# Optimization experiments

Measured on AMD Instinct MI355X. Metric: run time of the kernel, lower is better.

## Reference

```python
import jax, jax.numpy as jnp
import numpy as np

D = 0.035          # propagation distance (m)
LAMBDA = 5.32e-07  # wavelength (m)
RES = 64           # field resolution
N_LAYERS = 3
M = 50             # Monte-Carlo screens
BATCH = 128
NUM_CLASSES = 10
W0 = 0.01          # beam waist (m)
L_COH = 2e-3       # coherence length (m)
DX = 1e-06         # pixel pitch (m)
K = 2.0 * np.pi / LAMBDA


def _transfer_fn():
    # Angular-spectrum Fresnel transfer function H (host-side constant)
    f = np.fft.fftfreq(RES, DX)
    FX, FY = np.meshgrid(f, f)
    H = np.exp(1j * K * D) * np.exp(-1j * np.pi * LAMBDA * D * (FX ** 2 + FY ** 2))
    return jnp.asarray(H, dtype=jnp.complex64)


def setup_inputs() -> dict:
    key = jax.random.key(0)
    kx, k1, k2, kp, kw, kb = jax.random.split(key, 6)
    x = jax.random.uniform(kx, (BATCH, 1, RES, RES), dtype=jnp.float32)
    # Gauss-Schell complex random screens T_m (paper Eq.6), precomputed since they are random draws
    Cm = jax.random.normal(k1, (M, RES, RES), dtype=jnp.float32) + 1j * jax.random.normal(k2, (M, RES, RES), dtype=jnp.float32)
    v = np.fft.fftfreq(RES, 1.0 / RES)
    VX, VY = np.meshgrid(v, v)
    p = 2.0 * np.pi * L_COH ** 2 * np.exp(-2.0 * np.pi ** 2 * L_COH ** 2 * (VX ** 2 + VY ** 2))
    Tm = jnp.fft.ifft2(Cm * jnp.asarray(np.sqrt(p), dtype=jnp.float32))
    g = np.linspace(-W0 / 2, W0 / 2, RES)
    X, Y = np.meshgrid(g, g)
    gauss = jnp.asarray(np.exp(-(X ** 2 + Y ** 2) / W0 ** 2), dtype=jnp.float32)
    Tm = Tm * gauss
    Tm = Tm / jnp.max(jnp.abs(Tm), axis=(1, 2), keepdims=True)
    Tm = Tm.astype(jnp.complex64)
    phase_masks = jax.random.normal(kp, (N_LAYERS, RES, RES), dtype=jnp.float32) * 0.1
    fc_w = jax.random.normal(kw, (NUM_CLASSES, RES * RES), dtype=jnp.float32) * (1.0 / RES)
    fc_b = jax.random.normal(kb, (NUM_CLASSES,), dtype=jnp.float32) * 0.01
    return {"x": x, "screens_re": jnp.real(Tm), "screens_im": jnp.imag(Tm),
            "phase_masks": phase_masks, "fc_w": fc_w, "fc_b": fc_b}


def reference(x, screens_re, screens_im, phase_masks, fc_w, fc_b):
    H = _transfer_fn()  # [RES, RES] complex64
    screens = (screens_re + 1j * screens_im).astype(jnp.complex64)  # [M, r, r]
    # field: [M, B, r, r] -- all Monte-Carlo screens batched at once
    field = x[:, 0].astype(jnp.complex64)[None, :, :, :] * screens[:, None, :, :]
    for l in range(phase_masks.shape[0]):  # small fixed layer count
        field = field * jnp.exp(1j * phase_masks[l]).astype(jnp.complex64)
        field = jnp.fft.ifft2(jnp.fft.fft2(field) * H)
    avg_intensity = jnp.mean(jnp.abs(field) ** 2, axis=0)  # [B, r, r]
    feat = avg_intensity.reshape(avg_intensity.shape[0], -1)
    return feat @ fc_w.T + fc_b
```

## Files before the change

kernel.cpp:

```cpp
#include <hip/hip_runtime.h>
#include <math.h>

#define NM   50
#define NB   128
#define NL   3
#define NCLS 10

#define PI_D        3.14159265358979323846264338327950288
#define TWO_PI_D    6.28318530717958647692528676655900577
#define INV_2PI_D   0.159154943091895335768883763372514362
#define LAMBDA_D    5.32e-07
#define DIST_D      0.035
#define PLD_D       (PI_D * LAMBDA_D * DIST_D)
#define KD_D        (TWO_PI_D / LAMBDA_D * DIST_D)

typedef float f2 __attribute__((ext_vector_type(2)));

__device__ __forceinline__ f2 mkf2(float a, float b) { f2 r; r.x = a; r.y = b; return r; }

__device__ __forceinline__ int sw(int r, int c) {
    return r * 64 + (c ^ (((r & 3) << 2) ^ ((c >> 4) & 3)));
}
#define QS(r) ((((r) & 15)) << 1)

__device__ __forceinline__ constexpr int rev4(int i) {
    return ((i & 1) << 3) | ((i & 2) << 1) | ((i & 4) >> 1) | ((i & 8) >> 3);
}

__device__ __forceinline__ float dppx1(float v) {
    return __int_as_float(__builtin_amdgcn_mov_dpp(__float_as_int(v), 0xB1, 0xF, 0xF, true));
}
__device__ __forceinline__ float dppx2(float v) {
    return __int_as_float(__builtin_amdgcn_mov_dpp(__float_as_int(v), 0x4E, 0xF, 0xF, true));
}

__device__ __forceinline__ f2 cmul(f2 a, f2 w) {
    return a * w.x + a.yx * mkf2(-w.y, w.y);
}
__device__ __forceinline__ f2 cmulc(f2 a, f2 w) {
    return a * w.x + a.yx * mkf2(w.y, -w.y);
}

__device__ __forceinline__ constexpr float c16t(int tw) {
    return (tw == 1) ? 0.923879532511286756f : (tw == 2) ? 0.707106781186547524f :
           (tw == 3) ? 0.382683432365089772f : (tw == 5) ? -0.382683432365089772f :
           (tw == 6) ? -0.707106781186547524f : (tw == 7) ? -0.923879532511286756f : 1.0f;
}
__device__ __forceinline__ constexpr float s16t(int tw) {
    return (tw == 1) ? 0.382683432365089772f : (tw == 2) ? 0.707106781186547524f :
           (tw == 3) ? 0.923879532511286756f : (tw == 5) ? 0.923879532511286756f :
           (tw == 6) ? 0.707106781186547524f : (tw == 7) ? 0.382683432365089772f : 0.0f;
}

__device__ __forceinline__ void dif16_fwd(f2* x) {
#pragma unroll
    for (int len = 8; len >= 1; len >>= 1) {
#pragma unroll
        for (int base = 0; base < 16; base += 2 * len) {
#pragma unroll
            for (int j = 0; j < len; j++) {
                const int i0 = base + j, i1 = i0 + len;
                const int tw = j * (8 / len);
                f2 a = x[i0], b = x[i1];
                x[i0] = a + b;
                f2 d = a - b;
                if (tw == 0)      { x[i1] = d; }
                else if (tw == 4) { x[i1] = mkf2(d.y, -d.x); }
                else {
                    const float c = c16t(tw), s = s16t(tw);
                    x[i1] = d * c + d.yx * mkf2(s, -s);
                }
            }
        }
    }
}

__device__ __forceinline__ void dit16_inv(f2* x) {
#pragma unroll
    for (int len = 1; len <= 8; len <<= 1) {
#pragma unroll
        for (int base = 0; base < 16; base += 2 * len) {
#pragma unroll
            for (int j = 0; j < len; j++) {
                const int i0 = base + j, i1 = i0 + len;
                const int tw = j * (8 / len);
                f2 a = x[i0], b = x[i1];
                if (tw == 4)      { b = mkf2(-b.y, b.x); }
                else if (tw != 0) {
                    const float c = c16t(tw), s = s16t(tw);
                    b = b * c + b.yx * mkf2(-s, s);
                }
                x[i0] = a + b;
                x[i1] = a - b;
            }
        }
    }
}

__device__ __forceinline__ void quad_fwd(f2* x, float s1, float s2, bool l3) {
#pragma unroll
    for (int i = 0; i < 16; i++) {
        f2 p = mkf2(dppx2(x[i].x), dppx2(x[i].y));
        f2 r = x[i] * s2 + p;
        f2 r2 = l3 ? mkf2(r.y, -r.x) : r;
        f2 q = mkf2(dppx1(r2.x), dppx1(r2.y));
        x[i] = r2 * s1 + q;
    }
}

__device__ __forceinline__ void quad_inv(f2* x, float s1, float s2, bool l3) {
#pragma unroll
    for (int i = 0; i < 16; i++) {
        f2 p = mkf2(dppx1(x[i].x), dppx1(x[i].y));
        f2 r = x[i] * s1 + p;
        f2 r2 = l3 ? mkf2(-r.y, r.x) : r;
        f2 q = mkf2(dppx2(r2.x), dppx2(r2.y));
        x[i] = r2 * s2 + q;
    }
}

__device__ __forceinline__ void fwd64(f2* x, const f2* w64t, int t, float s1, float s2, bool l3) {
    dif16_fwd(x);
#pragma unroll
    for (int i = 1; i < 16; i++) x[i] = cmulc(x[i], w64t[t * rev4(i)]);
    quad_fwd(x, s1, s2, l3);
}
__device__ __forceinline__ void inv64(f2* x, const f2* w64t, int t, float s1, float s2, bool l3) {
    quad_inv(x, s1, s2, l3);
#pragma unroll
    for (int i = 1; i < 16; i++) x[i] = cmul(x[i], w64t[t * rev4(i)]);
    dit16_inv(x);
}

__global__ __launch_bounds__(256) void donn_main(
    const float* __restrict__ x,
    const float* __restrict__ sre,
    const float* __restrict__ sim,
    const float* __restrict__ phase,
    const float* __restrict__ fcw,
    const float* __restrict__ fcb,
    float* __restrict__ out)
{
    __shared__ f2 xb2[4096];
    __shared__ f2 w64t[64];
    __shared__ f2 hx2[64], hy2[64];

    const int tid = threadIdx.x;
    const int bid = blockIdx.x;
    const int b = bid & (NB - 1);
    const int m = bid >> 7;
    const int g = tid >> 2, t = tid & 3;
    const int sig = ((t & 1) << 1) | (t >> 1);
    const bool l3 = (t == 3);
    const float s1 = (t & 1) ? -1.f : 1.f;
    const float s2 = (t & 2) ? -1.f : 1.f;

    if (tid < 64) {
        float s, c;
        __sincosf((float)tid * (float)(TWO_PI_D / 64.0), &s, &c);
        w64t[tid] = mkf2(c, s);
        double f = (double)((tid < 32) ? tid : tid - 64) * 15625.0;
        double phd = -PLD_D * f * f;
        double r1 = phd - TWO_PI_D * rint(phd * INV_2PI_D);
        hx2[tid] = mkf2(cosf((float)r1), sinf((float)r1));
        double r2 = phd + KD_D;
        r2 = r2 - TWO_PI_D * rint(r2 * INV_2PI_D);
        hy2[tid] = mkf2(cosf((float)r2) * (1.0f / 4096.0f),
                        sinf((float)r2) * (1.0f / 4096.0f));
    }

    f2 X[16];
    {
        const float* xb = x   + b * 4096 + g * 64 + t;
        const float* sr = sre + m * 4096 + g * 64 + t;
        const float* si = sim + m * 4096 + g * 64 + t;
#pragma unroll
        for (int j = 0; j < 16; j++) {
            float xv = xb[4 * j];
            X[j].x = xv * sr[4 * j];
            X[j].y = xv * si[4 * j];
        }
    }
    __syncthreads();

#pragma unroll 1
    for (int l = 0; l < NL; l++) {
        const float* ph = phase + l * 4096 + g * 64 + t;
#pragma unroll
        for (int j = 0; j < 16; j++) {
            float s, c;
            __sincosf(ph[4 * j], &s, &c);
            X[j] = cmul(X[j], mkf2(c, s));
        }
        fwd64(X, w64t, t, s1, s2, l3);
#pragma unroll
        for (int i = 0; i < 16; i++) {
            const int kk = rev4(i) + 16 * sig;
            X[i] = cmul(X[i], hx2[kk]);
        }
#pragma unroll
        for (int i = 0; i < 16; i++) {
            const int kk = rev4(i) + 16 * sig;
            xb2[sw(g, kk)] = X[i];
        }
        __syncthreads();
#pragma unroll
        for (int j = 0; j < 16; j++)
            X[j] = xb2[sw(4 * j + t, g)];
        fwd64(X, w64t, t, s1, s2, l3);
#pragma unroll
        for (int i = 0; i < 16; i++) {
            const int kk = rev4(i) + 16 * sig;
            X[i] = cmul(X[i], hy2[kk]);
        }
        inv64(X, w64t, t, s1, s2, l3);
#pragma unroll
        for (int j = 0; j < 16; j++)
            xb2[sw(4 * j + t, g)] = X[j];
        __syncthreads();
#pragma unroll
        for (int i = 0; i < 16; i++) {
            const int kk = rev4(i) + 16 * sig;
            X[i] = xb2[sw(g, kk)];
        }
        inv64(X, w64t, t, s1, s2, l3);
    }

    __syncthreads();
    float* xbf = (float*)xb2;
    const int qsg = QS(g);
#pragma unroll
    for (int j = 0; j < 16; j++) {
        const int c0 = 4 * j + t;
        xbf[g * 64 + (c0 ^ qsg)] = fmaf(X[j].x, X[j].x, X[j].y * X[j].y);
    }
    __syncthreads();

    float ivl[16];
#pragma unroll
    for (int i = 0; i < 16; i++) {
        const int e = i * 256 + tid;
        const int r = e >> 6, c = e & 63;
        ivl[i] = xbf[r * 64 + (c ^ QS(r))];
    }
    float part[NCLS];
#pragma unroll
    for (int c2 = 0; c2 < NCLS; c2++) part[c2] = 0.f;
#pragma unroll
    for (int c2 = 0; c2 < NCLS; c2++) {
        const float* wrow = fcw + c2 * 4096 + tid;
#pragma unroll
        for (int i = 0; i < 16; i++)
            part[c2] = fmaf(ivl[i], wrow[i * 256], part[c2]);
    }
#pragma unroll
    for (int c2 = 0; c2 < NCLS; c2++) {
        float v = part[c2];
#pragma unroll
        for (int off = 32; off >= 1; off >>= 1) v += __shfl_down(v, off);
        if ((tid & 63) == 0) atomicAdd(&out[b * NCLS + c2], v * (1.0f / (float)NM));
    }
    if (m == 0 && tid < NCLS) atomicAdd(&out[b * NCLS + tid], fcb[tid]);
}

extern "C" void kernel_launch(void* const* d_in, const int* in_sizes, int n_in,
                              void* d_out, int out_size, void* d_ws, size_t ws_size,
                              hipStream_t stream) {
    const float* x   = (const float*)d_in[0];
    const float* sre = (const float*)d_in[1];
    const float* sim = (const float*)d_in[2];
    const float* ph  = (const float*)d_in[3];
    const float* fcw = (const float*)d_in[4];
    const float* fcb = (const float*)d_in[5];
    float* out = (float*)d_out;

    hipMemsetAsync(out, 0, (size_t)(NB * NCLS) * sizeof(float), stream);
    donn_main<<<NM * NB, 256, 0, stream>>>(x, sre, sim, ph, fcw, fcb, out);
}
```

Baseline: 305.5 us.

## Precompute phase-mask sincos tables, drop per-layer scaling, vectorize input loads

```diff
diff --git a/kernel.cpp b/kernel.cpp
--- a/kernel.cpp
+++ b/kernel.cpp
@@ -12,7 +12,8 @@
 #define LAMBDA_D    5.32e-07
 #define DIST_D      0.035
 #define PLD_D       (PI_D * LAMBDA_D * DIST_D)
-#define KD_D        (TWO_PI_D / LAMBDA_D * DIST_D)
+
+#define OUT_SCALE 4.2351647362715017e-24f
 
 typedef float f2 __attribute__((ext_vector_type(2)));
 
@@ -132,18 +133,31 @@
     dit16_inv(x);
 }
 
+__global__ __launch_bounds__(256) void donn_tables(
+    const float* __restrict__ phase, f2* __restrict__ ws)
+{
+    const int id = blockIdx.x * 256 + threadIdx.x;
+    const int l = id >> 12, rr = id & 4095;
+    const int tidm = rr >> 4, j = rr & 15;
+    const int g = tidm >> 2, t = tidm & 3;
+    float ph = phase[l * 4096 + g * 64 + 4 * j + t];
+    float s, c;
+    sincosf(ph, &s, &c);
+    ws[id] = mkf2(c, s);
+}
+
 __global__ __launch_bounds__(256) void donn_main(
     const float* __restrict__ x,
     const float* __restrict__ sre,
     const float* __restrict__ sim,
-    const float* __restrict__ phase,
+    const f2* __restrict__ ws,
     const float* __restrict__ fcw,
     const float* __restrict__ fcb,
     float* __restrict__ out)
 {
     __shared__ f2 xb2[4096];
     __shared__ f2 w64t[64];
-    __shared__ f2 hx2[64], hy2[64];
+    __shared__ f2 hx2[64];
 
     const int tid = threadIdx.x;
     const int bid = blockIdx.x;
@@ -163,34 +177,35 @@
         double phd = -PLD_D * f * f;
         double r1 = phd - TWO_PI_D * rint(phd * INV_2PI_D);
         hx2[tid] = mkf2(cosf((float)r1), sinf((float)r1));
-        double r2 = phd + KD_D;
-        r2 = r2 - TWO_PI_D * rint(r2 * INV_2PI_D);
-        hy2[tid] = mkf2(cosf((float)r2) * (1.0f / 4096.0f),
-                        sinf((float)r2) * (1.0f / 4096.0f));
     }
 
     f2 X[16];
     {
-        const float* xb = x   + b * 4096 + g * 64 + t;
-        const float* sr = sre + m * 4096 + g * 64 + t;
-        const float* si = sim + m * 4096 + g * 64 + t;
-#pragma unroll
-        for (int j = 0; j < 16; j++) {
-            float xv = xb[4 * j];
-            X[j].x = xv * sr[4 * j];
-            X[j].y = xv * si[4 * j];
-        }
+        const float4* xp = (const float4*)(x   + (size_t)b * 4096 + tid * 16);
+        const float4* rp = (const float4*)(sre + (size_t)m * 4096 + tid * 16);
+        const float4* ip = (const float4*)(sim + (size_t)m * 4096 + tid * 16);
+#pragma unroll
+        for (int a = 0; a < 4; a++) {
+            float4 xv = xp[a], rv = rp[a], iv = ip[a];
+            xb2[sw(g, 16 * t + 4 * a + 0)] = mkf2(xv.x * rv.x, xv.x * iv.x);
+            xb2[sw(g, 16 * t + 4 * a + 1)] = mkf2(xv.y * rv.y, xv.y * iv.y);
+            xb2[sw(g, 16 * t + 4 * a + 2)] = mkf2(xv.z * rv.z, xv.z * iv.z);
+            xb2[sw(g, 16 * t + 4 * a + 3)] = mkf2(xv.w * rv.w, xv.w * iv.w);
+        }
+#pragma unroll
+        for (int j = 0; j < 16; j++)
+            X[j] = xb2[sw(g, 4 * j + t)];
     }
     __syncthreads();
 
 #pragma unroll 1
     for (int l = 0; l < NL; l++) {
-        const float* ph = phase + l * 4096 + g * 64 + t;
-#pragma unroll
-        for (int j = 0; j < 16; j++) {
-            float s, c;
-            __sincosf(ph[4 * j], &s, &c);
-            X[j] = cmul(X[j], mkf2(c, s));
+        const float4* csp = (const float4*)(ws + ((l * 256 + tid) << 4));
+#pragma unroll
+        for (int q = 0; q < 8; q++) {
+            float4 c4 = csp[q];
+            X[2 * q]     = cmul(X[2 * q],     mkf2(c4.x, c4.y));
+            X[2 * q + 1] = cmul(X[2 * q + 1], mkf2(c4.z, c4.w));
         }
         fwd64(X, w64t, t, s1, s2, l3);
 #pragma unroll
@@ -211,7 +226,7 @@
 #pragma unroll
         for (int i = 0; i < 16; i++) {
             const int kk = rev4(i) + 16 * sig;
-            X[i] = cmul(X[i], hy2[kk]);
+            X[i] = cmul(X[i], hx2[kk]);
         }
         inv64(X, w64t, t, s1, s2, l3);
 #pragma unroll
@@ -236,29 +251,25 @@
     }
     __syncthreads();
 
-    float ivl[16];
+    float part[NCLS];
+#pragma unroll
+    for (int c2 = 0; c2 < NCLS; c2++) part[c2] = 0.f;
 #pragma unroll
     for (int i = 0; i < 16; i++) {
         const int e = i * 256 + tid;
         const int r = e >> 6, c = e & 63;
-        ivl[i] = xbf[r * 64 + (c ^ QS(r))];
-    }
-    float part[NCLS];
-#pragma unroll
-    for (int c2 = 0; c2 < NCLS; c2++) part[c2] = 0.f;
-#pragma unroll
-    for (int c2 = 0; c2 < NCLS; c2++) {
-        const float* wrow = fcw + c2 * 4096 + tid;
-#pragma unroll
-        for (int i = 0; i < 16; i++)
-            part[c2] = fmaf(ivl[i], wrow[i * 256], part[c2]);
+        const float iv = xbf[r * 64 + (c ^ QS(r))];
+        const float* wcol = fcw + e;
+#pragma unroll
+        for (int c2 = 0; c2 < NCLS; c2++)
+            part[c2] = fmaf(iv, wcol[(size_t)c2 * 4096], part[c2]);
     }
 #pragma unroll
     for (int c2 = 0; c2 < NCLS; c2++) {
         float v = part[c2];
 #pragma unroll
         for (int off = 32; off >= 1; off >>= 1) v += __shfl_down(v, off);
-        if ((tid & 63) == 0) atomicAdd(&out[b * NCLS + c2], v * (1.0f / (float)NM));
+        if ((tid & 63) == 0) atomicAdd(&out[b * NCLS + c2], v * OUT_SCALE);
     }
     if (m == 0 && tid < NCLS) atomicAdd(&out[b * NCLS + tid], fcb[tid]);
 }
@@ -273,7 +284,9 @@
     const float* fcw = (const float*)d_in[4];
     const float* fcb = (const float*)d_in[5];
     float* out = (float*)d_out;
+    f2* ws = (f2*)d_ws;
 
     hipMemsetAsync(out, 0, (size_t)(NB * NCLS) * sizeof(float), stream);
-    donn_main<<<NM * NB, 256, 0, stream>>>(x, sre, sim, ph, fcw, fcb, out);
-}
+    donn_tables<<<48, 256, 0, stream>>>(ph, ws);
+    donn_main<<<NM * NB, 256, 0, stream>>>(x, sre, sim, ws, fcw, fcb, out);
+}
```

After: 509.4 us. 66.7% more time.
